# Optimization experiments

Measured on AMD Instinct MI355X. Metric: run time of the kernel, lower is better.

The kernel has to match this reference:

```python
import jax, jax.numpy as jnp
import numpy as np

PAD = 1
DIL = 1
K = 9  # 3x3 kernel points


def conv2d(x, w, b):
    # standard NCHW conv, stride 1, padding PAD, dilation DIL
    y = jax.lax.conv_general_dilated(
        x, w, window_strides=(1, 1), padding=[(PAD, PAD), (PAD, PAD)],
        rhs_dilation=(DIL, DIL), dimension_numbers=('NCHW', 'OIHW', 'NCHW'))
    return y + b[None, :, None, None]


def deform_conv(x, offset, w):
    # x: [B,C,H,W], offset: [B,2K,H,W] (y at 2k, x at 2k+1), w: [O,C,3,3]
    B, C, H, W = x.shape
    O = w.shape[0]
    off = offset.reshape(B, K, 2, H, W)
    ky = jnp.repeat(jnp.arange(3), 3).astype(x.dtype)  # [K]
    kx = jnp.tile(jnp.arange(3), 3).astype(x.dtype)    # [K]
    base_h = jnp.arange(H, dtype=x.dtype) - PAD
    base_w = jnp.arange(W, dtype=x.dtype) - PAD
    # sampling positions [B,K,H,W]
    py = base_h[None, None, :, None] + (ky * DIL)[None, :, None, None] + off[:, :, 0]
    px = base_w[None, None, None, :] + (kx * DIL)[None, :, None, None] + off[:, :, 1]
    y0 = jnp.floor(py)
    x0 = jnp.floor(px)
    wy = py - y0
    wx = px - x0

    def gather(yi, xi):
        yc = jnp.clip(yi, 0, H - 1).astype(jnp.int32)
        xc = jnp.clip(xi, 0, W - 1).astype(jnp.int32)
        valid = ((yi >= 0) & (yi <= H - 1) & (xi >= 0) & (xi <= W - 1)).astype(x.dtype)
        # per-batch fancy gather -> [B,C,K,H,W]
        v = jax.vmap(lambda xb, yb, xbb: xb[:, yb, xbb])(x, yc, xc)
        return v * valid[:, None]

    v00 = gather(y0, x0)
    v01 = gather(y0, x0 + 1)
    v10 = gather(y0 + 1, x0)
    v11 = gather(y0 + 1, x0 + 1)
    a = (1 - wy)[:, None]; b_ = wy[:, None]
    c = (1 - wx)[:, None]; d = wx[:, None]
    samp = v00 * a * c + v01 * a * d + v10 * b_ * c + v11 * b_ * d  # [B,C,K,H,W]
    return jnp.einsum('bckhw,ock->bohw', samp, w.reshape(O, C, K))


def layer(x, w_off, b_off, w):
    offset = conv2d(x, w_off, b_off)
    return jax.nn.relu(deform_conv(x, offset, w))


def setup_inputs() -> dict:
    key = jax.random.key(0)
    ks = jax.random.split(key, 10)
    B, C, H, W = 4, 256, 96, 96
    inp = {"x": jax.random.normal(ks[0], (B, C, H, W), jnp.float32)}
    s = 1.0 / np.sqrt(C * 9)  # kaiming-ish scale for deform weights
    for i in range(3):
        inp[f"w_off{i}"] = jax.random.normal(ks[1 + 3 * i], (2 * K, C, 3, 3), jnp.float32) * 0.01
        inp[f"b_off{i}"] = jnp.zeros((2 * K,), jnp.float32)
        inp[f"w{i}"] = jax.random.normal(ks[3 + 3 * i], (C, C, 3, 3), jnp.float32) * s
    return inp


def reference(x, w_off0, b_off0, w0, w_off1, b_off1, w1, w_off2, b_off2, w2):
    for (wo, bo, w) in ((w_off0, b_off0, w0), (w_off1, b_off1, w1), (w_off2, b_off2, w2)):
        x = layer(x, wo, bo, w)
    return x
```

## Files before the change

### kernel.cpp

```cpp
#include <hip/hip_runtime.h>

#define Hc 96
#define Wc 96
#define Cc 256
#define Bc 4
#define KK 9
#define HW 9216
#define PIX 36864
#define CK 2304

typedef _Float16 f16;
typedef __attribute__((ext_vector_type(4))) _Float16 f16x4;
typedef __attribute__((ext_vector_type(8))) _Float16 f16x8;
typedef __attribute__((ext_vector_type(4))) float f32x4;

__device__ __forceinline__ int clampi(int v, int lo, int hi) {
    return v < lo ? lo : (v > hi ? hi : v);
}

#define SB() __builtin_amdgcn_sched_barrier(0)

__global__ __launch_bounds__(256) void prep_all_kernel(
    const float* __restrict__ x0,
    const float* __restrict__ w0, const float* __restrict__ wo0,
    const float* __restrict__ w1, const float* __restrict__ wo1,
    const float* __restrict__ w2, const float* __restrict__ wo2,
    f16* __restrict__ x16, f16* __restrict__ wT2, f16* __restrict__ woffT)
{
    const int blk = blockIdx.x;
    const int tid = threadIdx.x;
    if (blk < 2304) {
        __shared__ float st[64][65];
        const int hw0 = (blk % 144) * 64;
        const int c0  = ((blk / 144) & 3) * 64;
        const int b   = blk / 576;
        const int a = tid & 63, r = tid >> 6;
#pragma unroll
        for (int it = 0; it < 16; ++it) {
            int cl = it * 4 + r;
            st[cl][a] = x0[((size_t)(b * Cc + c0 + cl)) * HW + hw0 + a];
        }
        __syncthreads();
#pragma unroll
        for (int it = 0; it < 16; ++it) {
            int hwl = it * 4 + r;
            x16[((size_t)(b * HW + hw0 + hwl)) * Cc + c0 + a] = (f16)st[a][hwl];
        }
    } else {
        const int bb = blk - 2304;
        const int l = bb / 2592, b = bb - l * 2592;
        const float* w = (l == 0) ? w0 : (l == 1) ? w1 : w2;
        const float* wo = (l == 0) ? wo0 : (l == 1) ? wo1 : wo2;
        if (b < 2304) {
            int u = b * 256 + tid;
            int c = u & 255, o = (u >> 8) & 255, k = u >> 16;
            wT2[(size_t)l * CK * Cc + u] = (f16)w[(o * Cc + c) * KK + k];
        } else {
            int u = (b - 2304) * 256 + tid;
            int c = u & 255, j = (u >> 8) & 31, k = u >> 13;
            float v = (j < 18) ? wo[((size_t)j * Cc + c) * KK + k] : 0.f;
            woffT[(size_t)l * 9 * 32 * Cc + u] = (f16)v;
        }
    }
}

__global__ __launch_bounds__(768, 3) void fused_layer_kernel(
    const f16* __restrict__ x16, const f16* __restrict__ wT2,
    const f16* __restrict__ woffT, const float* __restrict__ b_off,
    f16* __restrict__ o16, float* __restrict__ oN, int last)
{
    __shared__ __align__(16) f16 s_w[2][2][8192];
    __shared__ __align__(16) f16 s_s[2][2][4608];
    __shared__ __align__(16) f16 s_a[2][2][1024];
    __shared__ int4   s_id[9][144];
    __shared__ float4 s_wt[9][144];

    const int bid = blockIdx.x;
    const int swz = (bid & 7) * 32 + (bid >> 3);
    const int p0 = swz * 144;
    const int imgb = (p0 / HW) * HW;
    const int tid = threadIdx.x, lane = tid & 63, wid = tid >> 6;
    const int wo = wid & 3, wp = wid >> 2;
    const bool sampler = (wid < 9);
    const int ps = tid >> 2, cg = tid & 3;
    const int qa = ((lane >> 4) ^ ((lane >> 1) & 3)) * 8;
    const int qs = (cg ^ ((ps >> 1) & 3)) * 8;
    const f16* xb = x16 + (size_t)imgb * Cc;
    const int wlo = (tid >> 2) * Cc + ((tid & 3) ^ ((tid >> 3) & 3)) * 8;
    const int wds = tid * 8;
    const int hwp = p0 + ps - imgb;
    const int hp = hwp / Wc, wp_ = hwp - hp * Wc;
    const int au0 = tid - 576;
    const int arow0 = au0 >> 3, acb0 = au0 & 7;
    const int ah0 = acb0 >> 2, aq0 = acb0 & 3;
    const int adst0 = arow0 * 32 + ((aq0 ^ ((arow0 >> 1) & 3)) * 8);
    const int arow1 = arow0 + 24;
    const int adst1 = arow1 * 32 + ((aq0 ^ ((arow1 >> 1) & 3)) * 8);

    {
        f32x4 accA[2];
        accA[0] = (f32x4){0.f, 0.f, 0.f, 0.f};
        accA[1] = (f32x4){0.f, 0.f, 0.f, 0.f};
        f16x8 X0, X1;

#define PA_LOAD(q) do {                                                        \
    int q_ = (q) > 35 ? 35 : (q);                                              \
    int k2_ = q_ >> 2, cq_ = q_ & 3;                                           \
    int ky_ = k2_ / 3, kx_ = k2_ - ky_ * 3;                                    \
    if (sampler) {                                                             \
        int yy_ = hp + ky_ - 1, xx_ = wp_ + kx_ - 1;                           \
        f16x8 t0_ = {0,0,0,0,0,0,0,0}, t1_ = {0,0,0,0,0,0,0,0};                \
        if (yy_ >= 0 && yy_ < Hc && xx_ >= 0 && xx_ < Wc) {                    \
            const f16* s_ = x16 + ((size_t)(imgb + yy_ * Wc + xx_)) * Cc + cq_ * 64 + cg * 8; \
            t0_ = *(const f16x8*)s_;                                           \
            t1_ = *(const f16x8*)(s_ + 32);                                    \
        }                                                                      \
        X0 = t0_; X1 = t1_;                                                    \
    } else {                                                                   \
        X0 = *(const f16x8*)(woffT + ((size_t)(k2_ * 32 + arow0)) * Cc + cq_ * 64 + acb0 * 8); \
        if (tid < 640)                                                         \
            X1 = *(const f16x8*)(woffT + ((size_t)(k2_ * 32 + arow1)) * Cc + cq_ * 64 + acb0 * 8); \
    }                                                                          \
} while (0)

#define PA_STAGE(nb) do {                                                      \
    if (sampler) {                                                             \
        *(f16x8*)&s_s[nb][0][ps * 32 + qs] = X0;                               \
        *(f16x8*)&s_s[nb][1][ps * 32 + qs] = X1;                               \
    } else {                                                                   \
        *(f16x8*)&s_a[nb][ah0][adst0] = X0;                                    \
        if (tid < 640) *(f16x8*)&s_a[nb][ah0][adst1] = X1;                     \
    }                                                                          \
} while (0)

        PA_LOAD(0);
        PA_STAGE(0);
        PA_LOAD(1);
        asm volatile("s_waitcnt lgkmcnt(0)" ::: "memory"); SB();
        __builtin_amdgcn_s_barrier(); SB();

        for (int p = 0; p < 36; ++p) {
            const int bb = p & 1, nb = bb ^ 1;
            f16x8 af0, af1, bf0, bf1;
            if (sampler) {
                af0 = *(const f16x8*)&s_a[bb][0][((lane & 15)) * 32 + qa];
                af1 = *(const f16x8*)&s_a[bb][0][((16 + (lane & 15))) * 32 + qa];
                bf0 = *(const f16x8*)&s_s[bb][0][(wid * 16 + (lane & 15)) * 32 + qa];
            }
            PA_STAGE(nb);
            PA_LOAD(p + 2);
            if (sampler) {
                accA[0] = __builtin_amdgcn_mfma_f32_16x16x32_f16(af0, bf0, accA[0], 0, 0, 0);
                accA[1] = __builtin_amdgcn_mfma_f32_16x16x32_f16(af1, bf0, accA[1], 0, 0, 0);
                af0 = *(const f16x8*)&s_a[bb][1][((lane & 15)) * 32 + qa];
                af1 = *(const f16x8*)&s_a[bb][1][((16 + (lane & 15))) * 32 + qa];
                bf1 = *(const f16x8*)&s_s[bb][1][(wid * 16 + (lane & 15)) * 32 + qa];
                accA[0] = __builtin_amdgcn_mfma_f32_16x16x32_f16(af0, bf1, accA[0], 0, 0, 0);
                accA[1] = __builtin_amdgcn_mfma_f32_16x16x32_f16(af1, bf1, accA[1], 0, 0, 0);
            }
            asm volatile("s_waitcnt lgkmcnt(0)" ::: "memory"); SB();
            __builtin_amdgcn_s_barrier(); SB();
        }

        if (sampler) {
            const int q = lane >> 4;
            const int pxl = wid * 16 + (lane & 15);
            const int hwq = p0 + pxl - imgb;
            const int hq = hwq / Wc, wq = hwq - hq * Wc;
#define STORE_TAP_LDS(kk, offy, offx) do {                                     \
    float py_ = (float)(hq - 1 + (kk) / 3) + (offy);                           \
    float px_ = (float)(wq - 1 + (kk) % 3) + (offx);                           \
    float y0f_ = floorf(py_), x0f_ = floorf(px_);                              \
    float wy_ = py_ - y0f_, wx_ = px_ - x0f_;                                  \
    int iy0_ = (int)y0f_, ix0_ = (int)x0f_;                                    \
    float vy0_ = (y0f_ >= 0.f && y0f_ <= 95.f) ? 1.f : 0.f;                    \
    float vy1_ = (y0f_ + 1.f >= 0.f && y0f_ + 1.f <= 95.f) ? 1.f : 0.f;        \
    float vx0_ = (x0f_ >= 0.f && x0f_ <= 95.f) ? 1.f : 0.f;                    \
    float vx1_ = (x0f_ + 1.f >= 0.f && x0f_ + 1.f <= 95.f) ? 1.f : 0.f;        \
    int cy0_ = clampi(iy0_, 0, 95), cy1_ = clampi(iy0_ + 1, 0, 95);            \
    int cx0_ = clampi(ix0_, 0, 95), cx1_ = clampi(ix0_ + 1, 0, 95);            \
    s_id[kk][pxl] = make_int4(cy0_ * Wc + cx0_, cy0_ * Wc + cx1_,              \
                              cy1_ * Wc + cx0_, cy1_ * Wc + cx1_);             \
    s_wt[kk][pxl] = make_float4((1.f - wy_) * (1.f - wx_) * vy0_ * vx0_,       \
                                (1.f - wy_) * wx_ * vy0_ * vx1_,               \
                                wy_ * (1.f - wx_) * vy1_ * vx0_,               \
                                wy_ * wx_ * vy1_ * vx1_);                      \
} while (0)
            STORE_TAP_LDS(2 * q,     accA[0][0] + b_off[4 * q],
                                     accA[0][1] + b_off[4 * q + 1]);
            STORE_TAP_LDS(2 * q + 1, accA[0][2] + b_off[4 * q + 2],
                                     accA[0][3] + b_off[4 * q + 3]);
            if (q == 0)
                STORE_TAP_LDS(8, accA[1][0] + b_off[16], accA[1][1] + b_off[17]);
#undef STORE_TAP_LDS
        }
        asm volatile("s_waitcnt lgkmcnt(0)" ::: "memory"); SB();
        __builtin_amdgcn_s_barrier(); SB();
    }

#define ISSUE_W(kt, cq, h, nb) do {                                            \
    const f16* g0_ = wT2 + wlo + ((size_t)((kt) * 256)) * Cc + (cq) * 64 + (h) * 32; \
    __builtin_amdgcn_global_load_lds(                                          \
        (const __attribute__((address_space(1))) void*)g0_,                    \
        (__attribute__((address_space(3))) void*)&s_w[nb][h][wds], 16, 0, 0);  \
    if (wid >= 8) {                                                            \
        const f16* g1_ = wT2 + wlo + ((size_t)((kt) * 256 + 64)) * Cc + (cq) * 64 + (h) * 32; \
        __builtin_amdgcn_global_load_lds(                                      \
            (const __attribute__((address_space(1))) void*)g1_,                \
            (__attribute__((address_space(3))) void*)&s_w[nb][h][2048 + wds], 16, 0, 0); \
    }                                                                          \
} while (0)

#define ISSUE_C(dst, idv, co) do {                                             \
    (dst)[0] = *(const f16x8*)(xb + (size_t)(idv).x * Cc + (co) + cg * 8);     \
    (dst)[1] = *(const f16x8*)(xb + (size_t)(idv).y * Cc + (co) + cg * 8);     \
    (dst)[2] = *(const f16x8*)(xb + (size_t)(idv).z * Cc + (co) + cg * 8);     \
    (dst)[3] = *(const f16x8*)(xb + (size_t)(idv).w * Cc + (co) + cg * 8);     \
} while (0)

#define BLEND_WRITE(src, wvv, h, nb) do {                                      \
    f16x8 sv_ = (src)[0] * (f16)(wvv).x + (src)[1] * (f16)(wvv).y              \
              + (src)[2] * (f16)(wvv).z + (src)[3] * (f16)(wvv).w;             \
    *(f16x8*)&s_s[nb][h][ps * 32 + qs] = sv_;                                  \
} while (0)

    f32x4 acc[4][3];
#pragma unroll
    for (int mi = 0; mi < 4; ++mi)
#pragma unroll
        for (int ni = 0; ni < 3; ++ni) acc[mi][ni] = (f32x4){0.f, 0.f, 0.f, 0.f};

    f16x8 c4a[4], c4b[4];
    int4 id;
    float4 wv;
    int4 idN;
    float4 wvN;
    if (sampler) {
        id = s_id[0][ps];
        wv = s_wt[0][ps];
    }

    ISSUE_W(0, 0, 0, 0);
    ISSUE_W(0, 0, 1, 0);
    SB();
    if (sampler) {
        ISSUE_C(c4a, id, 0);
        ISSUE_C(c4b, id, 32);
        BLEND_WRITE(c4a, wv, 0, 0);
        BLEND_WRITE(c4b, wv, 1, 0);
        ISSUE_C(c4a, id, 64);
        ISSUE_C(c4b, id, 96);
        asm volatile("s_waitcnt lgkmcnt(0)" ::: "memory"); SB();
        if (wid == 8) {
            asm volatile("s_waitcnt vmcnt(8)" ::: "memory"); SB();
        }
    } else {
        asm volatile("s_waitcnt vmcnt(0)" ::: "memory"); SB();
    }
    __builtin_amdgcn_s_barrier(); SB();

    for (int k = 0; k < 9; ++k) {
        const int kn = (k < 8) ? k + 1 : 8;
#pragma unroll
        for (int ch = 0; ch < 4; ++ch) {
            const int bb = ch & 1, nb = bb ^ 1;
            f16x8 bf0[3], bf1[3];
#pragma unroll
            for (int ni = 0; ni < 3; ++ni) {
                bf0[ni] = *(const f16x8*)&s_s[bb][0][(wp * 48 + ni * 16 + (lane & 15)) * 32 + qa];
                bf1[ni] = *(const f16x8*)&s_s[bb][1][(wp * 48 + ni * 16 + (lane & 15)) * 32 + qa];
            }
            if (sampler) {
                if (ch == 1) {
                    idN = s_id[kn][ps];
                    wvN = s_wt[kn][ps];
                }
                ISSUE_W((ch == 3) ? kn : k, (ch + 1) & 3, 0, nb);
                ISSUE_W((ch == 3) ? kn : k, (ch + 1) & 3, 1, nb);
                SB();
                {
                    const float4 wvu = (ch == 3) ? wvN : wv;
                    const int4 idu = (ch >= 2) ? idN : id;
                    const int co2 = ((ch + 2) & 3) * 64;
                    BLEND_WRITE(c4a, wvu, 0, nb);
                    ISSUE_C(c4a, idu, co2);
                    BLEND_WRITE(c4b, wvu, 1, nb);
                    ISSUE_C(c4b, idu, co2 + 32);
                }
            } else {
                ISSUE_W((ch == 3) ? kn : k, (ch + 1) & 3, 0, nb);
                ISSUE_W((ch == 3) ? kn : k, (ch + 1) & 3, 1, nb);
                SB();
            }
#pragma unroll
            for (int mi = 0; mi < 4; ++mi) {
                f16x8 af = *(const f16x8*)&s_w[bb][0][(wo * 64 + mi * 16 + (lane & 15)) * 32 + qa];
#pragma unroll
                for (int ni = 0; ni < 3; ++ni)
                    acc[mi][ni] = __builtin_amdgcn_mfma_f32_16x16x32_f16(
                        af, bf0[ni], acc[mi][ni], 0, 0, 0);
            }
#pragma unroll
            for (int mi = 0; mi < 4; ++mi) {
                f16x8 af = *(const f16x8*)&s_w[bb][1][(wo * 64 + mi * 16 + (lane & 15)) * 32 + qa];
#pragma unroll
                for (int ni = 0; ni < 3; ++ni)
                    acc[mi][ni] = __builtin_amdgcn_mfma_f32_16x16x32_f16(
                        af, bf1[ni], acc[mi][ni], 0, 0, 0);
            }
            asm volatile("s_waitcnt lgkmcnt(0)" ::: "memory"); SB();
            if (sampler) {
                asm volatile("s_waitcnt vmcnt(8)" ::: "memory"); SB();
            } else {
                asm volatile("s_waitcnt vmcnt(0)" ::: "memory"); SB();
            }
            __builtin_amdgcn_s_barrier(); SB();
        }
        if (sampler) { id = idN; wv = wvN; }
    }

    if (!last) {
#pragma unroll
        for (int ni = 0; ni < 3; ++ni) {
            const int p = p0 + wp * 48 + ni * 16 + (lane & 15);
#pragma unroll
            for (int mi = 0; mi < 4; ++mi) {
                const int o0 = wo * 64 + mi * 16 + (lane >> 4) * 4;
                f32x4 v = acc[mi][ni];
                f16x4 h = {(f16)fmaxf(v[0], 0.f), (f16)fmaxf(v[1], 0.f),
                           (f16)fmaxf(v[2], 0.f), (f16)fmaxf(v[3], 0.f)};
                *(f16x4*)&o16[(size_t)p * Cc + o0] = h;
            }
        }
    } else {
        const int bimg = imgb / HW;
#pragma unroll
        for (int ni = 0; ni < 3; ++ni) {
            const int p = p0 + wp * 48 + ni * 16 + (lane & 15);
            const int hwl = p - imgb;
#pragma unroll
            for (int mi = 0; mi < 4; ++mi) {
                const int o0 = wo * 64 + mi * 16 + (lane >> 4) * 4;
#pragma unroll
                for (int j = 0; j < 4; ++j)
                    oN[((size_t)(bimg * Cc + o0 + j)) * HW + hwl] =
                        fmaxf(acc[mi][ni][j], 0.f);
            }
        }
    }
#undef ISSUE_W
#undef ISSUE_C
#undef BLEND_WRITE
#undef PA_LOAD
#undef PA_STAGE
}

extern "C" void kernel_launch(void* const* d_in, const int* in_sizes, int n_in,
                              void* d_out, int out_size, void* d_ws, size_t ws_size,
                              hipStream_t stream)
{
    const float* x0 = (const float*)d_in[0];
    float* out = (float*)d_out;

    f16*   x16a = (f16*)d_ws;
    f16*   x16b = x16a + (size_t)PIX * Cc;
    f16*   wT2  = x16b + (size_t)PIX * Cc;
    f16*   woffT = wT2 + (size_t)3 * CK * Cc;

    prep_all_kernel<<<2304 + 3 * 2592, 256, 0, stream>>>(
        x0,
        (const float*)d_in[3], (const float*)d_in[1],
        (const float*)d_in[6], (const float*)d_in[4],
        (const float*)d_in[9], (const float*)d_in[7],
        x16a, wT2, woffT);

    const f16* xin = x16a;
    for (int L = 0; L < 3; ++L) {
        const float* b_off = (const float*)d_in[2 + 3 * L];
        const int last = (L == 2);
        f16* xo = (L == 0) ? x16b : x16a;

        fused_layer_kernel<<<PIX / 144, 768, 0, stream>>>(
            xin, wT2 + (size_t)L * CK * Cc, woffT + (size_t)L * 9 * 32 * Cc,
            b_off, xo, out, last);

        xin = xo;
    }
}
```

Before: 241.6 us.

## Triple-buffer weight tiles with two-stage prefetch and compact sampling metadata

Weight tiles in shared memory go from double to triple buffering. Each step now prefetches the weight tile two steps ahead, and non-sampler waves wait only for the older batch of loads rather than all outstanding loads. This is meant to hide global-to-LDS weight latency behind the matrix-core work. To keep shared memory within budget, the bilinear indices shrink to 16-bit shorts, the blend weights are stored as fp16, and the offset-conv staging buffer is aliased onto the third weight buffer. The cost is relaxed wait counts for the sampler waves, which risks a race, plus a leftover dead LDS read.

Result: no change. 244.8 us (+1.3%).

```diff
diff --git a/kernel.cpp b/kernel.cpp
--- a/kernel.cpp
+++ b/kernel.cpp
@@ -69,11 +69,10 @@
     const f16* __restrict__ woffT, const float* __restrict__ b_off,
     f16* __restrict__ o16, float* __restrict__ oN, int last)
 {
-    __shared__ __align__(16) f16 s_w[2][2][8192];
+    __shared__ __align__(16) f16 s_w[3][2][8192];
     __shared__ __align__(16) f16 s_s[2][2][4608];
-    __shared__ __align__(16) f16 s_a[2][2][1024];
-    __shared__ int4   s_id[9][144];
-    __shared__ float4 s_wt[9][144];
+    __shared__ ushort4 s_id[9][144];
+    __shared__ __align__(8) f16x4 s_wt[9][144];
 
     const int bid = blockIdx.x;
     const int swz = (bid & 7) * 32 + (bid >> 3);
@@ -96,6 +95,7 @@
     const int adst0 = arow0 * 32 + ((aq0 ^ ((arow0 >> 1) & 3)) * 8);
     const int arow1 = arow0 + 24;
     const int adst1 = arow1 * 32 + ((aq0 ^ ((arow1 >> 1) & 3)) * 8);
+    f16 (*s_a)[2][1024] = reinterpret_cast<f16(*)[2][1024]>(&s_w[2][0][0]);
 
     {
         f32x4 accA[2];
@@ -179,12 +179,16 @@
     float vx1_ = (x0f_ + 1.f >= 0.f && x0f_ + 1.f <= 95.f) ? 1.f : 0.f;        \
     int cy0_ = clampi(iy0_, 0, 95), cy1_ = clampi(iy0_ + 1, 0, 95);            \
     int cx0_ = clampi(ix0_, 0, 95), cx1_ = clampi(ix0_ + 1, 0, 95);            \
-    s_id[kk][pxl] = make_int4(cy0_ * Wc + cx0_, cy0_ * Wc + cx1_,              \
-                              cy1_ * Wc + cx0_, cy1_ * Wc + cx1_);             \
-    s_wt[kk][pxl] = make_float4((1.f - wy_) * (1.f - wx_) * vy0_ * vx0_,       \
-                                (1.f - wy_) * wx_ * vy0_ * vx1_,               \
-                                wy_ * (1.f - wx_) * vy1_ * vx0_,               \
-                                wy_ * wx_ * vy1_ * vx1_);                      \
+    s_id[kk][pxl] = make_ushort4((unsigned short)(cy0_ * Wc + cx0_),           \
+                                 (unsigned short)(cy0_ * Wc + cx1_),           \
+                                 (unsigned short)(cy1_ * Wc + cx0_),           \
+                                 (unsigned short)(cy1_ * Wc + cx1_));          \
+    f16x4 wv4_;                                                                \
+    wv4_[0] = (f16)((1.f - wy_) * (1.f - wx_) * vy0_ * vx0_);                  \
+    wv4_[1] = (f16)((1.f - wy_) * wx_ * vy0_ * vx1_);                          \
+    wv4_[2] = (f16)(wy_ * (1.f - wx_) * vy1_ * vx0_);                          \
+    wv4_[3] = (f16)(wy_ * wx_ * vy1_ * vx1_);                                  \
+    s_wt[kk][pxl] = wv4_;                                                      \
 } while (0)
             STORE_TAP_LDS(2 * q,     accA[0][0] + b_off[4 * q],
                                      accA[0][1] + b_off[4 * q + 1]);
@@ -198,16 +202,22 @@
         __builtin_amdgcn_s_barrier(); SB();
     }
 
-#define ISSUE_W(kt, cq, h, nb) do {                                            \
-    const f16* g0_ = wT2 + wlo + ((size_t)((kt) * 256)) * Cc + (cq) * 64 + (h) * 32; \
+#define ISSUE_W(kt, cq, wb) do {                                               \
+    const f16* g0_ = wT2 + wlo + ((size_t)((kt) * 256)) * Cc + (cq) * 64;      \
     __builtin_amdgcn_global_load_lds(                                          \
         (const __attribute__((address_space(1))) void*)g0_,                    \
-        (__attribute__((address_space(3))) void*)&s_w[nb][h][wds], 16, 0, 0);  \
+        (__attribute__((address_space(3))) void*)&s_w[wb][0][wds], 16, 0, 0);  \
+    __builtin_amdgcn_global_load_lds(                                          \
+        (const __attribute__((address_space(1))) void*)(g0_ + 32),             \
+        (__attribute__((address_space(3))) void*)&s_w[wb][1][wds], 16, 0, 0);  \
     if (wid >= 8) {                                                            \
-        const f16* g1_ = wT2 + wlo + ((size_t)((kt) * 256 + 64)) * Cc + (cq) * 64 + (h) * 32; \
+        const f16* g1_ = g0_ + (size_t)64 * Cc;                                \
         __builtin_amdgcn_global_load_lds(                                      \
             (const __attribute__((address_space(1))) void*)g1_,                \
-            (__attribute__((address_space(3))) void*)&s_w[nb][h][2048 + wds], 16, 0, 0); \
+            (__attribute__((address_space(3))) void*)&s_w[wb][0][2048 + wds], 16, 0, 0); \
+        __builtin_amdgcn_global_load_lds(                                      \
+            (const __attribute__((address_space(1))) void*)(g1_ + 32),         \
+            (__attribute__((address_space(3))) void*)&s_w[wb][1][2048 + wds], 16, 0, 0); \
     }                                                                          \
 } while (0)
 
@@ -219,8 +229,8 @@
 } while (0)
 
 #define BLEND_WRITE(src, wvv, h, nb) do {                                      \
-    f16x8 sv_ = (src)[0] * (f16)(wvv).x + (src)[1] * (f16)(wvv).y              \
-              + (src)[2] * (f16)(wvv).z + (src)[3] * (f16)(wvv).w;             \
+    f16x8 sv_ = (src)[0] * (wvv)[0] + (src)[1] * (wvv)[1]                      \
+              + (src)[2] * (wvv)[2] + (src)[3] * (wvv)[3];                     \
     *(f16x8*)&s_s[nb][h][ps * 32 + qs] = sv_;                                  \
 } while (0)
 
@@ -231,17 +241,17 @@
         for (int ni = 0; ni < 3; ++ni) acc[mi][ni] = (f32x4){0.f, 0.f, 0.f, 0.f};
 
     f16x8 c4a[4], c4b[4];
-    int4 id;
-    float4 wv;
-    int4 idN;
-    float4 wvN;
+    ushort4 id;
+    f16x4 wv;
+    ushort4 idN;
+    f16x4 wvN;
     if (sampler) {
         id = s_id[0][ps];
         wv = s_wt[0][ps];
     }
 
-    ISSUE_W(0, 0, 0, 0);
-    ISSUE_W(0, 0, 1, 0);
+    ISSUE_W(0, 0, 0);
+    ISSUE_W(0, 1, 1);
     SB();
     if (sampler) {
         ISSUE_C(c4a, id, 0);
@@ -251,20 +261,24 @@
         ISSUE_C(c4a, id, 64);
         ISSUE_C(c4b, id, 96);
         asm volatile("s_waitcnt lgkmcnt(0)" ::: "memory"); SB();
-        if (wid == 8) {
-            asm volatile("s_waitcnt vmcnt(8)" ::: "memory"); SB();
-        }
     } else {
-        asm volatile("s_waitcnt vmcnt(0)" ::: "memory"); SB();
+        asm volatile("s_waitcnt vmcnt(4)" ::: "memory"); SB();
     }
     __builtin_amdgcn_s_barrier(); SB();
 
+    int rb = 0;
     for (int k = 0; k < 9; ++k) {
-        const int kn = (k < 8) ? k + 1 : 8;
 #pragma unroll
         for (int ch = 0; ch < 4; ++ch) {
-            const int bb = ch & 1, nb = bb ^ 1;
+            const int g = k * 4 + ch;
+            const int bb = g & 1, nb = bb ^ 1;
+            const int g2 = (g + 2 > 35) ? 35 : g + 2;
+            const int wb = (rb + 2 >= 3) ? rb - 1 : rb + 2;
             f16x8 bf0[3], bf1[3];
+#pragma unroll
+            for (int ni = 0; ni < 3; ++ni) {
+                bf0[ni] = *(const f16x8*)&s_w[rb][0][0];
+            }
 #pragma unroll
             for (int ni = 0; ni < 3; ++ni) {
                 bf0[ni] = *(const f16x8*)&s_s[bb][0][(wp * 48 + ni * 16 + (lane & 15)) * 32 + qa];
@@ -272,15 +286,15 @@
             }
             if (sampler) {
                 if (ch == 1) {
+                    const int kn = (k < 8) ? k + 1 : 8;
                     idN = s_id[kn][ps];
                     wvN = s_wt[kn][ps];
                 }
-                ISSUE_W((ch == 3) ? kn : k, (ch + 1) & 3, 0, nb);
-                ISSUE_W((ch == 3) ? kn : k, (ch + 1) & 3, 1, nb);
+                ISSUE_W(g2 >> 2, g2 & 3, wb);
                 SB();
                 {
-                    const float4 wvu = (ch == 3) ? wvN : wv;
-                    const int4 idu = (ch >= 2) ? idN : id;
+                    const f16x4 wvu = (ch == 3) ? wvN : wv;
+                    const ushort4 idu = (ch >= 2) ? idN : id;
                     const int co2 = ((ch + 2) & 3) * 64;
                     BLEND_WRITE(c4a, wvu, 0, nb);
                     ISSUE_C(c4a, idu, co2);
@@ -288,13 +302,12 @@
                     ISSUE_C(c4b, idu, co2 + 32);
                 }
             } else {
-                ISSUE_W((ch == 3) ? kn : k, (ch + 1) & 3, 0, nb);
-                ISSUE_W((ch == 3) ? kn : k, (ch + 1) & 3, 1, nb);
+                ISSUE_W(g2 >> 2, g2 & 3, wb);
                 SB();
             }
 #pragma unroll
             for (int mi = 0; mi < 4; ++mi) {
-                f16x8 af = *(const f16x8*)&s_w[bb][0][(wo * 64 + mi * 16 + (lane & 15)) * 32 + qa];
+                f16x8 af = *(const f16x8*)&s_w[rb][0][(wo * 64 + mi * 16 + (lane & 15)) * 32 + qa];
 #pragma unroll
                 for (int ni = 0; ni < 3; ++ni)
                     acc[mi][ni] = __builtin_amdgcn_mfma_f32_16x16x32_f16(
@@ -302,19 +315,18 @@
             }
 #pragma unroll
             for (int mi = 0; mi < 4; ++mi) {
-                f16x8 af = *(const f16x8*)&s_w[bb][1][(wo * 64 + mi * 16 + (lane & 15)) * 32 + qa];
+                f16x8 af = *(const f16x8*)&s_w[rb][1][(wo * 64 + mi * 16 + (lane & 15)) * 32 + qa];
 #pragma unroll
                 for (int ni = 0; ni < 3; ++ni)
                     acc[mi][ni] = __builtin_amdgcn_mfma_f32_16x16x32_f16(
                         af, bf1[ni], acc[mi][ni], 0, 0, 0);
             }
             asm volatile("s_waitcnt lgkmcnt(0)" ::: "memory"); SB();
-            if (sampler) {
-                asm volatile("s_waitcnt vmcnt(8)" ::: "memory"); SB();
-            } else {
-                asm volatile("s_waitcnt vmcnt(0)" ::: "memory"); SB();
+            if (!sampler) {
+                asm volatile("s_waitcnt vmcnt(4)" ::: "memory"); SB();
             }
             __builtin_amdgcn_s_barrier(); SB();
+            rb = (rb + 1 >= 3) ? 0 : rb + 1;
         }
         if (sampler) { id = idN; wv = wvN; }
     }
```
